# Kernel tuning notes

Hardware: AMD Instinct MI355X
Metric: run time of the kernel (lower is better)

Reference implementation:

```python
import jax, jax.numpy as jnp
import numpy as np

EPS = 1e-7


def setup_inputs() -> dict:
    key = jax.random.key(0)
    k1, k2, k3 = jax.random.split(key, 3)
    B, IN, OUT = 256, 256, 512
    x = jax.random.uniform(k1, (B, IN), dtype=jnp.float32)
    w = jax.random.uniform(k2, (IN, OUT), dtype=jnp.float32)
    t = jax.random.uniform(k3, (B, OUT), dtype=jnp.float32)
    return {"x": x, "w": w, "t": t}


def reference(x, w, t):
    # x: [B, IN], w: [IN, OUT], t: [B, OUT]
    xe = x[:, :, None]          # [B, IN, 1]
    te = t[:, None, :]          # [B, 1, OUT]
    we = w[None, :, :]          # [1, IN, OUT]

    one = jnp.asarray(1.0, dtype=x.dtype)
    # rel_x: relevance of x, reduced over batch dim 0 -> [1, IN, OUT]
    rel_x = jnp.minimum(te / (xe + EPS), one).sum(axis=0, keepdims=True) \
            / xe.sum(axis=0, keepdims=True)
    # rel_w: relevance of w, reduced over IN dim -> [B, 1, OUT]
    rel_w = jnp.minimum(te / (we + EPS), one).sum(axis=-2, keepdims=True) \
            / xe.sum(axis=-2, keepdims=True)

    ind_x = jnp.argmax(xe * rel_x, axis=-2, keepdims=True)  # [B, 1, OUT]
    ind_w = jnp.argmax(rel_w * we, axis=-2, keepdims=True)  # [B, 1, OUT]

    inner_x = xe * jax.lax.stop_gradient(we)  # [B, IN, OUT]
    inner_w = jax.lax.stop_gradient(xe) * we  # [B, IN, OUT]

    chosen_x = jnp.take_along_axis(inner_x, ind_x, axis=-2).squeeze(-2)  # [B, OUT]
    chosen_w = jnp.take_along_axis(inner_w, ind_w, axis=-2).squeeze(-2)  # [B, OUT]
    return chosen_x, chosen_w
```

## Files before the change

### kernel.cpp

```cpp
#include <hip/hip_runtime.h>

constexpr int B   = 256;
constexpr int IN  = 256;
constexpr int OUT = 512;
constexpr double EPSD = 1e-7;

typedef unsigned long long ull;


__global__ __launch_bounds__(256) void k_setup(const float* __restrict__ x,
        double* __restrict__ rxd, double* __restrict__ part, float* __restrict__ xt) {
    const int tid = threadIdx.x;
    const int blk = blockIdx.x;
    if (blk < 32) {
        const int b0 = blk * 8;
        #pragma unroll
        for (int k = 0; k < 8; ++k)
            rxd[(b0 + k) * IN + tid] = 1.0 / ((double)x[(b0 + k) * IN + tid] + EPSD);
    } else if (blk < 40) {
        const int j = blk - 32, b0 = j * 32;
        double s0 = 0, s1 = 0, s2 = 0, s3 = 0;
        #pragma unroll
        for (int k = 0; k < 32; k += 4) {
            s0 += (double)x[(b0 + k + 0) * IN + tid];
            s1 += (double)x[(b0 + k + 1) * IN + tid];
            s2 += (double)x[(b0 + k + 2) * IN + tid];
            s3 += (double)x[(b0 + k + 3) * IN + tid];
        }
        part[j * IN + tid] = (s0 + s1) + (s2 + s3);
    } else {
        __shared__ float tile[64][65];
        const int tl  = blk - 40;
        const int tr0 = (tl >> 2) * 64;
        const int tc0 = (tl & 3) * 64;
        const int c   = tid & 63;
        const int r4  = tid >> 6;
        #pragma unroll
        for (int k = 0; k < 16; ++k) {
            const int r = r4 + k * 4;
            tile[r][c] = x[(tr0 + r) * IN + tc0 + c];
        }
        __syncthreads();
        #pragma unroll
        for (int k = 0; k < 16; ++k) {
            const int r = r4 + k * 4;
            xt[(size_t)(tc0 + r) * B + tr0 + c] = tile[c][r];
        }
    }
}

__global__ __launch_bounds__(512, 4) void k_main(const float* __restrict__ w,
        const float* __restrict__ t, const double* __restrict__ rxd,
        const double* __restrict__ part, const float* __restrict__ xt,
        float* __restrict__ out) {
    const int tid = threadIdx.x;
    const int j   = tid & 255;
    const int o   = blockIdx.x;

    __shared__ double tc[B];
    __shared__ double rcs[IN];
    __shared__ double rp[4][IN];
    __shared__ double rc[IN];
    __shared__ ull    keys[4][B];
    __shared__ ull    swv[4];

    int warg_o = 0;
    if (tid < 256) {
        tc[j] = (double)t[j * OUT + o];
        double ps = 0.0;
        #pragma unroll
        for (int k = 0; k < 8; ++k) ps += part[k * IN + j];
        rcs[j] = 1.0 / ps;
        float wv = w[j * OUT + o];
        ull key = ((ull)__float_as_uint(wv) << 8) | (unsigned)(255 - j);
        #pragma unroll
        for (int off = 32; off; off >>= 1) {
            ull v = __shfl_down(key, off);
            key = v > key ? v : key;
        }
        if ((tid & 63) == 0) swv[tid >> 6] = key;
    }
    __syncthreads();
    if (tid < 256) {
        ull wk = swv[0];
        #pragma unroll
        for (int k = 1; k < 4; ++k) { ull v = swv[k]; wk = v > wk ? v : wk; }
        warg_o = 255 - (int)(wk & 0xFFull);
    }

    {
        const int i0 = (tid & 127) * 2;
        const int bq = tid >> 7;
        const double* __restrict__ tcc  = tc + bq * 64;
        const double* __restrict__ base = rxd + (size_t)(bq * 64) * IN + i0;
        double a0 = 0, a1 = 0, a2 = 0, a3 = 0;
        #pragma unroll 8
        for (int k = 0; k < 64; k += 2) {
            double2 r0 = *(const double2*)(base + (size_t)k * IN);
            double2 r1 = *(const double2*)(base + (size_t)(k + 1) * IN);
            double t0 = tcc[k], t1 = tcc[k + 1];
            a0 += fmin(t0 * r0.x, 1.0);
            a1 += fmin(t0 * r0.y, 1.0);
            a2 += fmin(t1 * r1.x, 1.0);
            a3 += fmin(t1 * r1.y, 1.0);
        }
        rp[bq][i0]     = a0 + a2;
        rp[bq][i0 + 1] = a1 + a3;
    }
    __syncthreads();
    if (tid < 256)
        rc[j] = (((rp[0][j] + rp[1][j]) + (rp[2][j] + rp[3][j]))) * rcs[j];
    __syncthreads();

    {
        const int b0 = (tid & 127) * 2;
        const int iq = tid >> 7;
        double mA0 = -1.0, mA1 = -1.0, mB0 = -1.0, mB1 = -1.0;
        #pragma unroll 8
        for (int i = iq * 64; i < iq * 64 + 64; i += 2) {
            float2 x0 = *(const float2*)&xt[(size_t)i * B + b0];
            float2 x1 = *(const float2*)&xt[(size_t)(i + 1) * B + b0];
            double s00 = (double)x0.x * rc[i];
            double s01 = (double)x0.y * rc[i];
            double s10 = (double)x1.x * rc[i + 1];
            double s11 = (double)x1.y * rc[i + 1];
            long long u00 = (__double_as_longlong(s00) & ~0xFFll) | (long long)(255 - i);
            long long u01 = (__double_as_longlong(s01) & ~0xFFll) | (long long)(255 - i);
            long long u10 = (__double_as_longlong(s10) & ~0xFFll) | (long long)(255 - (i + 1));
            long long u11 = (__double_as_longlong(s11) & ~0xFFll) | (long long)(255 - (i + 1));
            mA0 = fmax(mA0, __longlong_as_double(u00));
            mB0 = fmax(mB0, __longlong_as_double(u01));
            mA1 = fmax(mA1, __longlong_as_double(u10));
            mB1 = fmax(mB1, __longlong_as_double(u11));
        }
        keys[iq][b0]     = (ull)__double_as_longlong(fmax(mA0, mA1));
        keys[iq][b0 + 1] = (ull)__double_as_longlong(fmax(mB0, mB1));
    }
    __syncthreads();

    if (tid < 256) {
        const int b = j;
        ull mk = keys[0][b];
        #pragma unroll
        for (int k = 1; k < 4; ++k) { ull v = keys[k][b]; mk = v > mk ? v : mk; }
        const int ia = 255 - (int)(mk & 0xFFull);

        float* __restrict__ out0 = out;
        float* __restrict__ out1 = out + (size_t)B * OUT;
        out0[b * OUT + o] = xt[(size_t)ia * B + b] * w[ia * OUT + o];

        const int iw = (tc[b] > 0.0) ? warg_o : 0;
        out1[b * OUT + o] = xt[(size_t)iw * B + b] * w[iw * OUT + o];
    }
}

extern "C" void kernel_launch(void* const* d_in, const int* in_sizes, int n_in,
                              void* d_out, int out_size, void* d_ws, size_t ws_size,
                              hipStream_t stream) {
    const float* x = (const float*)d_in[0];
    const float* w = (const float*)d_in[1];
    const float* t = (const float*)d_in[2];
    float* out = (float*)d_out;

    double* dws  = (double*)d_ws;
    double* RXD  = dws;
    double* PART = RXD + (size_t)B * IN;
    float*  XT   = (float*)(PART + 8 * IN);

    k_setup<<<56, 256, 0, stream>>>(x, RXD, PART, XT);
    k_main<<<OUT, 512, 0, stream>>>(w, t, RXD, PART, XT, out);
}
```

Measured before the change: 82.74 us.

## Process two output columns per block and pre-transpose t and w

Each k_main block now handles two output columns, so every rxd and xt load from global memory is reused for two columns' relevance sums and argmax scans. The setup kernel also transposes t and w into workspace, which turns the per-column strided reads into coalesced ones. In exchange the grid is halved to 256 blocks, register pressure rises (launch bounds lowered to 2), and the setup kernel gains extra transpose blocks.

Result: slower. 85.52 us (+3.4%).

```diff
diff --git a/kernel.cpp b/kernel.cpp
--- a/kernel.cpp
+++ b/kernel.cpp
@@ -9,7 +9,9 @@
 
 
 __global__ __launch_bounds__(256) void k_setup(const float* __restrict__ x,
-        double* __restrict__ rxd, double* __restrict__ part, float* __restrict__ xt) {
+        const float* __restrict__ t, const float* __restrict__ w,
+        double* __restrict__ rxd, double* __restrict__ part,
+        float* __restrict__ xt, float* __restrict__ tt, float* __restrict__ wt) {
     const int tid = threadIdx.x;
     const int blk = blockIdx.x;
     if (blk < 32) {
@@ -30,127 +32,161 @@
         part[j * IN + tid] = (s0 + s1) + (s2 + s3);
     } else {
         __shared__ float tile[64][65];
-        const int tl  = blk - 40;
-        const int tr0 = (tl >> 2) * 64;
-        const int tc0 = (tl & 3) * 64;
-        const int c   = tid & 63;
-        const int r4  = tid >> 6;
+        const int c  = tid & 63;
+        const int r4 = tid >> 6;
+        const float* src; float* dst; int scols, srows_t0, scols_t0, dcols;
+        if (blk < 56) {
+            const int tl = blk - 40;
+            src = x;  dst = xt;  scols = IN; dcols = B;
+            srows_t0 = (tl >> 2) * 64;  scols_t0 = (tl & 3) * 64;
+        } else if (blk < 88) {
+            const int tl = blk - 56;
+            src = t;  dst = tt;  scols = OUT; dcols = B;
+            srows_t0 = (tl >> 3) * 64;  scols_t0 = (tl & 7) * 64;
+        } else {
+            const int tl = blk - 88;
+            src = w;  dst = wt;  scols = OUT; dcols = IN;
+            srows_t0 = (tl >> 3) * 64;  scols_t0 = (tl & 7) * 64;
+        }
         #pragma unroll
         for (int k = 0; k < 16; ++k) {
             const int r = r4 + k * 4;
-            tile[r][c] = x[(tr0 + r) * IN + tc0 + c];
+            tile[r][c] = src[(srows_t0 + r) * scols + scols_t0 + c];
         }
         __syncthreads();
         #pragma unroll
         for (int k = 0; k < 16; ++k) {
             const int r = r4 + k * 4;
-            xt[(size_t)(tc0 + r) * B + tr0 + c] = tile[c][r];
+            dst[(size_t)(scols_t0 + r) * dcols + srows_t0 + c] = tile[c][r];
         }
     }
 }
 
-__global__ __launch_bounds__(512, 4) void k_main(const float* __restrict__ w,
-        const float* __restrict__ t, const double* __restrict__ rxd,
+__global__ __launch_bounds__(512, 2) void k_main(const float* __restrict__ wt,
+        const float* __restrict__ tt, const double* __restrict__ rxd,
         const double* __restrict__ part, const float* __restrict__ xt,
         float* __restrict__ out) {
-    const int tid = threadIdx.x;
-    const int j   = tid & 255;
-    const int o   = blockIdx.x;
-
-    __shared__ double tc[B];
+    const int tid  = threadIdx.x;
+    const int half = tid >> 8;
+    const int j    = tid & 255;
+    const int o0   = blockIdx.x * 2;
+    const int o    = o0 + half;
+
+    __shared__ double tc[2][B];
     __shared__ double rcs[IN];
-    __shared__ double rp[4][IN];
-    __shared__ double rc[IN];
-    __shared__ ull    keys[4][B];
-    __shared__ ull    swv[4];
-
-    int warg_o = 0;
+    __shared__ double rp[2][4][IN];
+    __shared__ double rc[2][IN];
+    __shared__ ull    keys[2][4][B];
+    __shared__ ull    swv[2][4];
+
+    tc[half][j] = (double)tt[(size_t)o * B + j];
     if (tid < 256) {
-        tc[j] = (double)t[j * OUT + o];
         double ps = 0.0;
         #pragma unroll
         for (int k = 0; k < 8; ++k) ps += part[k * IN + j];
         rcs[j] = 1.0 / ps;
-        float wv = w[j * OUT + o];
+    }
+    {
+        float wv = wt[(size_t)o * IN + j];
         ull key = ((ull)__float_as_uint(wv) << 8) | (unsigned)(255 - j);
         #pragma unroll
         for (int off = 32; off; off >>= 1) {
             ull v = __shfl_down(key, off);
             key = v > key ? v : key;
         }
-        if ((tid & 63) == 0) swv[tid >> 6] = key;
-    }
-    __syncthreads();
-    if (tid < 256) {
-        ull wk = swv[0];
-        #pragma unroll
-        for (int k = 1; k < 4; ++k) { ull v = swv[k]; wk = v > wk ? v : wk; }
-        warg_o = 255 - (int)(wk & 0xFFull);
-    }
+        if ((tid & 63) == 0) swv[half][(tid >> 6) & 3] = key;
+    }
+    __syncthreads();
+    const int warg_o = [&]{
+        ull wk = swv[half][0];
+        #pragma unroll
+        for (int k = 1; k < 4; ++k) { ull v = swv[half][k]; wk = v > wk ? v : wk; }
+        return 255 - (int)(wk & 0xFFull);
+    }();
 
     {
         const int i0 = (tid & 127) * 2;
         const int bq = tid >> 7;
-        const double* __restrict__ tcc  = tc + bq * 64;
+        const double* __restrict__ t0c  = tc[0] + bq * 64;
+        const double* __restrict__ t1c  = tc[1] + bq * 64;
         const double* __restrict__ base = rxd + (size_t)(bq * 64) * IN + i0;
         double a0 = 0, a1 = 0, a2 = 0, a3 = 0;
+        double c0 = 0, c1 = 0, c2 = 0, c3 = 0;
         #pragma unroll 8
         for (int k = 0; k < 64; k += 2) {
             double2 r0 = *(const double2*)(base + (size_t)k * IN);
             double2 r1 = *(const double2*)(base + (size_t)(k + 1) * IN);
-            double t0 = tcc[k], t1 = tcc[k + 1];
-            a0 += fmin(t0 * r0.x, 1.0);
-            a1 += fmin(t0 * r0.y, 1.0);
-            a2 += fmin(t1 * r1.x, 1.0);
-            a3 += fmin(t1 * r1.y, 1.0);
-        }
-        rp[bq][i0]     = a0 + a2;
-        rp[bq][i0 + 1] = a1 + a3;
-    }
-    __syncthreads();
-    if (tid < 256)
-        rc[j] = (((rp[0][j] + rp[1][j]) + (rp[2][j] + rp[3][j]))) * rcs[j];
+            double ta0 = t0c[k], ta1 = t0c[k + 1];
+            double tb0 = t1c[k], tb1 = t1c[k + 1];
+            a0 += fmin(ta0 * r0.x, 1.0);
+            a1 += fmin(ta0 * r0.y, 1.0);
+            a2 += fmin(ta1 * r1.x, 1.0);
+            a3 += fmin(ta1 * r1.y, 1.0);
+            c0 += fmin(tb0 * r0.x, 1.0);
+            c1 += fmin(tb0 * r0.y, 1.0);
+            c2 += fmin(tb1 * r1.x, 1.0);
+            c3 += fmin(tb1 * r1.y, 1.0);
+        }
+        rp[0][bq][i0]     = a0 + a2;
+        rp[0][bq][i0 + 1] = a1 + a3;
+        rp[1][bq][i0]     = c0 + c2;
+        rp[1][bq][i0 + 1] = c1 + c3;
+    }
+    __syncthreads();
+    rc[half][j] = ((rp[half][0][j] + rp[half][1][j]) +
+                   (rp[half][2][j] + rp[half][3][j])) * rcs[j];
     __syncthreads();
 
     {
         const int b0 = (tid & 127) * 2;
         const int iq = tid >> 7;
+        const double* __restrict__ r0c = rc[0];
+        const double* __restrict__ r1c = rc[1];
         double mA0 = -1.0, mA1 = -1.0, mB0 = -1.0, mB1 = -1.0;
+        double nA0 = -1.0, nA1 = -1.0, nB0 = -1.0, nB1 = -1.0;
         #pragma unroll 8
         for (int i = iq * 64; i < iq * 64 + 64; i += 2) {
             float2 x0 = *(const float2*)&xt[(size_t)i * B + b0];
             float2 x1 = *(const float2*)&xt[(size_t)(i + 1) * B + b0];
-            double s00 = (double)x0.x * rc[i];
-            double s01 = (double)x0.y * rc[i];
-            double s10 = (double)x1.x * rc[i + 1];
-            double s11 = (double)x1.y * rc[i + 1];
-            long long u00 = (__double_as_longlong(s00) & ~0xFFll) | (long long)(255 - i);
-            long long u01 = (__double_as_longlong(s01) & ~0xFFll) | (long long)(255 - i);
-            long long u10 = (__double_as_longlong(s10) & ~0xFFll) | (long long)(255 - (i + 1));
-            long long u11 = (__double_as_longlong(s11) & ~0xFFll) | (long long)(255 - (i + 1));
-            mA0 = fmax(mA0, __longlong_as_double(u00));
-            mB0 = fmax(mB0, __longlong_as_double(u01));
-            mA1 = fmax(mA1, __longlong_as_double(u10));
-            mB1 = fmax(mB1, __longlong_as_double(u11));
-        }
-        keys[iq][b0]     = (ull)__double_as_longlong(fmax(mA0, mA1));
-        keys[iq][b0 + 1] = (ull)__double_as_longlong(fmax(mB0, mB1));
-    }
-    __syncthreads();
-
-    if (tid < 256) {
+            const long long e0 = (long long)(255 - i), e1 = (long long)(255 - (i + 1));
+            double s;
+            s = (double)x0.x * r0c[i];
+            mA0 = fmax(mA0, __longlong_as_double((__double_as_longlong(s) & ~0xFFll) | e0));
+            s = (double)x0.y * r0c[i];
+            mB0 = fmax(mB0, __longlong_as_double((__double_as_longlong(s) & ~0xFFll) | e0));
+            s = (double)x1.x * r0c[i + 1];
+            mA1 = fmax(mA1, __longlong_as_double((__double_as_longlong(s) & ~0xFFll) | e1));
+            s = (double)x1.y * r0c[i + 1];
+            mB1 = fmax(mB1, __longlong_as_double((__double_as_longlong(s) & ~0xFFll) | e1));
+            s = (double)x0.x * r1c[i];
+            nA0 = fmax(nA0, __longlong_as_double((__double_as_longlong(s) & ~0xFFll) | e0));
+            s = (double)x0.y * r1c[i];
+            nB0 = fmax(nB0, __longlong_as_double((__double_as_longlong(s) & ~0xFFll) | e0));
+            s = (double)x1.x * r1c[i + 1];
+            nA1 = fmax(nA1, __longlong_as_double((__double_as_longlong(s) & ~0xFFll) | e1));
+            s = (double)x1.y * r1c[i + 1];
+            nB1 = fmax(nB1, __longlong_as_double((__double_as_longlong(s) & ~0xFFll) | e1));
+        }
+        keys[0][iq][b0]     = (ull)__double_as_longlong(fmax(mA0, mA1));
+        keys[0][iq][b0 + 1] = (ull)__double_as_longlong(fmax(mB0, mB1));
+        keys[1][iq][b0]     = (ull)__double_as_longlong(fmax(nA0, nA1));
+        keys[1][iq][b0 + 1] = (ull)__double_as_longlong(fmax(nB0, nB1));
+    }
+    __syncthreads();
+
+    {
         const int b = j;
-        ull mk = keys[0][b];
-        #pragma unroll
-        for (int k = 1; k < 4; ++k) { ull v = keys[k][b]; mk = v > mk ? v : mk; }
+        ull mk = keys[half][0][b];
+        #pragma unroll
+        for (int k = 1; k < 4; ++k) { ull v = keys[half][k][b]; mk = v > mk ? v : mk; }
         const int ia = 255 - (int)(mk & 0xFFull);
 
         float* __restrict__ out0 = out;
         float* __restrict__ out1 = out + (size_t)B * OUT;
-        out0[b * OUT + o] = xt[(size_t)ia * B + b] * w[ia * OUT + o];
-
-        const int iw = (tc[b] > 0.0) ? warg_o : 0;
-        out1[b * OUT + o] = xt[(size_t)iw * B + b] * w[iw * OUT + o];
+        out0[b * OUT + o] = xt[(size_t)ia * B + b] * wt[(size_t)o * IN + ia];
+
+        const int iw = (tc[half][b] > 0.0) ? warg_o : 0;
+        out1[b * OUT + o] = xt[(size_t)iw * B + b] * wt[(size_t)o * IN + iw];
     }
 }
 
@@ -166,7 +202,9 @@
     double* RXD  = dws;
     double* PART = RXD + (size_t)B * IN;
     float*  XT   = (float*)(PART + 8 * IN);
-
-    k_setup<<<56, 256, 0, stream>>>(x, RXD, PART, XT);
-    k_main<<<OUT, 512, 0, stream>>>(w, t, RXD, PART, XT, out);
+    float*  TT   = XT + (size_t)IN * B;
+    float*  WT   = TT + (size_t)OUT * B;
+
+    k_setup<<<120, 256, 0, stream>>>(x, t, w, RXD, PART, XT, TT, WT);
+    k_main<<<OUT / 2, 512, 0, stream>>>(WT, TT, RXD, PART, XT, out);
 }
```
